# Performance work log

Hardware: AMD Instinct MI355X
Metric: run time of the kernel (lower is better)

The kernel has to match this reference:

```python
import jax, jax.numpy as jnp
import numpy as np

N_NODES = 50000
N_EDGES = 800000
IN, HID, OUT = 128, 128, 64


def _mean_agg(h, src, dst, n):
    # gather source-node features along edges, segment-mean into destination nodes
    msgs = h[src]                                          # [E, d]
    summ = jax.ops.segment_sum(msgs, dst, num_segments=n)  # [N, d]
    deg = jax.ops.segment_sum(jnp.ones((src.shape[0],), h.dtype), dst, num_segments=n)
    return summ / jnp.maximum(deg, 1.0)[:, None]           # zero-in-degree -> 0


def _sage_layer(h, src, dst, W_self, W_neigh, b, n):
    # DGL SAGEConv mean: fc_self(h) + fc_neigh(mean_neigh(h)) + bias
    agg = _mean_agg(h, src, dst, n)
    return h @ W_self + agg @ W_neigh + b


def setup_inputs() -> dict:
    key = jax.random.key(0)
    ks = jax.random.split(key, 8)
    s = 1.0 / np.sqrt(IN)
    return {
        "feat": jax.random.normal(ks[0], (N_NODES, IN), jnp.float32),
        "src": jax.random.randint(ks[1], (N_EDGES,), 0, N_NODES, jnp.int64),
        "dst": jax.random.randint(ks[2], (N_EDGES,), 0, N_NODES, jnp.int64),
        "W_self1": jax.random.normal(ks[3], (IN, HID), jnp.float32) * s,
        "W_neigh1": jax.random.normal(ks[4], (IN, HID), jnp.float32) * s,
        "b1": jnp.zeros((HID,), jnp.float32),
        "W_self2": jax.random.normal(ks[5], (HID, OUT), jnp.float32) * (1.0 / np.sqrt(HID)),
        "W_neigh2": jax.random.normal(ks[6], (HID, OUT), jnp.float32) * (1.0 / np.sqrt(HID)),
        "b2": jnp.zeros((OUT,), jnp.float32),
    }


def reference(feat, src, dst, W_self1, W_neigh1, b1, W_self2, W_neigh2, b2):
    n = feat.shape[0]
    h = _sage_layer(feat, src, dst, W_self1, W_neigh1, b1, n)
    h = jax.nn.relu(h)  # dropout is identity in eval mode
    h = _sage_layer(h, src, dst, W_self2, W_neigh2, b2, n)
    return h
```

## Files before the change

### kernel.cpp

```cpp
#include <hip/hip_runtime.h>

#define N_NODES 50000
#define N_EDGES 800000

typedef unsigned short ushort_t;
typedef unsigned int uint_t;
typedef __attribute__((ext_vector_type(8))) short bf16x8;
typedef __attribute__((ext_vector_type(4))) float f32x4;

#define NB 196
#define BCAP 6144
#define SDEPTH 32
#define EPB 2048
#define NBLK_BUCKET ((N_EDGES + EPB - 1) / EPB)
#define NCVT4 (N_NODES * 128 / 4)

#define IOFF_ROWPTR  100000
#define IOFF_EIDX    150016
#define IOFF_BCNT    950528
#define UOFF_WT      1920000
#define UOFF_FEATB   2000000
#define UOFF_AGG1B   8400000
#define UOFF_H1B     14800000
#define UOFF_P2B     21200000

__device__ __forceinline__ float bf2f(uint_t u) {
    return __uint_as_float(u << 16);
}
__device__ __forceinline__ uint_t f2bf(float f) {
    uint_t x = __float_as_uint(f);
    return (x + 0x7FFFu + ((x >> 16) & 1u)) >> 16;
}

__global__ __launch_bounds__(256) void prep_kernel(const float* __restrict__ feat,
                                                   const float* __restrict__ Ws1,
                                                   const float* __restrict__ Wn1,
                                                   const float* __restrict__ Ws2,
                                                   const float* __restrict__ Wn2,
                                                   ushort_t* __restrict__ featb,
                                                   ushort_t* __restrict__ wT,
                                                   int* __restrict__ bcnt) {
    int i = blockIdx.x * 256 + threadIdx.x;
    if (i < NCVT4) {
        float4 v = ((const float4*)feat)[i];
        uint2 o;
        o.x = f2bf(v.x) | (f2bf(v.y) << 16);
        o.y = f2bf(v.z) | (f2bf(v.w) << 16);
        ((uint2*)featb)[i] = o;
        return;
    }
    int j = i - NCVT4;
    if (j < 49152) {
        float v;
        if (j < 16384) {
            int n = j >> 7, k = j & 127;
            v = Ws1[k * 128 + n];
        } else if (j < 32768) {
            int jj = j - 16384, n = jj >> 7, k = jj & 127;
            v = Wn1[k * 128 + n];
        } else if (j < 40960) {
            int jj = j - 32768, n = jj >> 7, k = jj & 127;
            v = Wn2[k * 64 + n];
        } else {
            int jj = j - 40960, n = jj >> 7, k = jj & 127;
            v = Ws2[k * 64 + n];
        }
        wT[j] = (ushort_t)f2bf(v);
        return;
    }
    int z = j - 49152;
    if (z < NB) bcnt[z] = 0;
}

__global__ __launch_bounds__(256) void bucket_kernel(const int* __restrict__ src,
                                                     const int* __restrict__ dst,
                                                     uint_t* __restrict__ bucket,
                                                     int* __restrict__ bcnt) {
    __shared__ uint_t stage[NB][SDEPTH];
    __shared__ int lcnt[NB];
    __shared__ int gbase[NB];
    int tid = threadIdx.x;
    for (int i = tid; i < NB; i += 256) lcnt[i] = 0;
    __syncthreads();
    int e0 = blockIdx.x * EPB;
#pragma unroll
    for (int it = 0; it < EPB / 256; ++it) {
        int e = e0 + it * 256 + tid;
        if (e < N_EDGES) {
            int d = dst[e], s = src[e];
            uint_t v = ((uint_t)d << 16) | (uint_t)s;
            int b = d >> 8;
            int slot = atomicAdd(&lcnt[b], 1);
            if (slot < SDEPTH) {
                stage[b][slot] = v;
            } else {
                int p = atomicAdd(&bcnt[b], 1);
                bucket[(long)b * BCAP + p] = v;
            }
        }
    }
    __syncthreads();
    if (tid < NB) {
        int n = min(lcnt[tid], SDEPTH);
        gbase[tid] = (n > 0) ? atomicAdd(&bcnt[tid], n) : 0;
    }
    __syncthreads();
    for (int s = tid; s < NB * SDEPTH; s += 256) {
        int b = s >> 5, i = s & (SDEPTH - 1);
        if (i < min(lcnt[b], SDEPTH))
            bucket[(long)b * BCAP + gbase[b] + i] = stage[b][i];
    }
}

__global__ __launch_bounds__(1024) void fill_bucket(const uint_t* __restrict__ bucket,
                                                    const int* __restrict__ bcnt,
                                                    int* __restrict__ rowptr,
                                                    ushort_t* __restrict__ eidx) {
    __shared__ int pref[256];
    __shared__ int hist[256];
    __shared__ int excl[256];
    __shared__ int fp[256];
    int b = blockIdx.x, tid = threadIdx.x;
    if (tid < 256) {
        pref[tid] = (tid < NB) ? bcnt[tid] : 0;
        hist[tid] = 0;
        fp[tid] = 0;
    }
    __syncthreads();
    for (int off = 1; off < 256; off <<= 1) {
        int t = 0;
        if (tid < 256 && tid >= off) t = pref[tid - off];
        __syncthreads();
        if (tid < 256) pref[tid] += t;
        __syncthreads();
    }
    int n = bcnt[b];
    int base = pref[b] - n;
    if (b == NB - 1 && tid == 0) rowptr[N_NODES] = pref[NB - 1];
    int nodebase = b << 8;
    const uint_t* bk = bucket + (long)b * BCAP;
    for (int i = tid; i < n; i += 1024) {
        int d = (int)(bk[i] >> 16) - nodebase;
        atomicAdd(&hist[d], 1);
    }
    __syncthreads();
    int v = 0;
    if (tid < 256) { v = hist[tid]; excl[tid] = v; }
    __syncthreads();
    for (int off = 1; off < 256; off <<= 1) {
        int t = 0;
        if (tid < 256 && tid >= off) t = excl[tid - off];
        __syncthreads();
        if (tid < 256) excl[tid] += t;
        __syncthreads();
    }
    if (tid < 256) {
        excl[tid] -= v;
        int node = nodebase + tid;
        if (node < N_NODES) rowptr[node] = base + excl[tid];
    }
    __syncthreads();
    for (int i = tid; i < n; i += 1024) {
        uint_t vv = bk[i];
        int d = (int)(vv >> 16) - nodebase;
        int off = atomicAdd(&fp[d], 1);
        eidx[base + excl[d] + off] = (ushort_t)(vv & 0xFFFFu);
    }
}

__global__ __launch_bounds__(256) void gather128_kernel(const int* __restrict__ rowptr,
                                                        const ushort_t* __restrict__ eidx,
                                                        const ushort_t* __restrict__ xb,
                                                        ushort_t* __restrict__ aggb) {
    int node = blockIdx.x * 4 + (threadIdx.x >> 6);
    int lane = threadIdx.x & 63;
    if (node >= N_NODES) return;
    int q = lane >> 4;
    int sl = lane & 15;
    int beg = rowptr[node], end = rowptr[node + 1];
    float acc[8];
#pragma unroll
    for (int j = 0; j < 8; ++j) acc[j] = 0.f;

    int e = beg;
    for (; e + 7 < end; e += 8) {
        int sA = eidx[e + q];
        int sB = eidx[e + 4 + q];
        uint4 vA = *(const uint4*)(xb + (long)sA * 128 + sl * 8);
        uint4 vB = *(const uint4*)(xb + (long)sB * 128 + sl * 8);
        acc[0] += bf2f(vA.x & 0xffffu); acc[1] += bf2f(vA.x >> 16);
        acc[2] += bf2f(vA.y & 0xffffu); acc[3] += bf2f(vA.y >> 16);
        acc[4] += bf2f(vA.z & 0xffffu); acc[5] += bf2f(vA.z >> 16);
        acc[6] += bf2f(vA.w & 0xffffu); acc[7] += bf2f(vA.w >> 16);
        acc[0] += bf2f(vB.x & 0xffffu); acc[1] += bf2f(vB.x >> 16);
        acc[2] += bf2f(vB.y & 0xffffu); acc[3] += bf2f(vB.y >> 16);
        acc[4] += bf2f(vB.z & 0xffffu); acc[5] += bf2f(vB.z >> 16);
        acc[6] += bf2f(vB.w & 0xffffu); acc[7] += bf2f(vB.w >> 16);
    }
    for (; e + 3 < end; e += 4) {
        int s = eidx[e + q];
        uint4 v = *(const uint4*)(xb + (long)s * 128 + sl * 8);
        acc[0] += bf2f(v.x & 0xffffu); acc[1] += bf2f(v.x >> 16);
        acc[2] += bf2f(v.y & 0xffffu); acc[3] += bf2f(v.y >> 16);
        acc[4] += bf2f(v.z & 0xffffu); acc[5] += bf2f(v.z >> 16);
        acc[6] += bf2f(v.w & 0xffffu); acc[7] += bf2f(v.w >> 16);
    }
    if (e + q < end) {
        int s = eidx[e + q];
        uint4 v = *(const uint4*)(xb + (long)s * 128 + sl * 8);
        acc[0] += bf2f(v.x & 0xffffu); acc[1] += bf2f(v.x >> 16);
        acc[2] += bf2f(v.y & 0xffffu); acc[3] += bf2f(v.y >> 16);
        acc[4] += bf2f(v.z & 0xffffu); acc[5] += bf2f(v.z >> 16);
        acc[6] += bf2f(v.w & 0xffffu); acc[7] += bf2f(v.w >> 16);
    }
#pragma unroll
    for (int j = 0; j < 8; ++j) {
        acc[j] += __shfl_xor(acc[j], 16);
        acc[j] += __shfl_xor(acc[j], 32);
    }
    float inv = (end > beg) ? 1.0f / (float)(end - beg) : 0.f;
    if (lane < 16) {
        uint4 o;
        o.x = f2bf(acc[0] * inv) | (f2bf(acc[1] * inv) << 16);
        o.y = f2bf(acc[2] * inv) | (f2bf(acc[3] * inv) << 16);
        o.z = f2bf(acc[4] * inv) | (f2bf(acc[5] * inv) << 16);
        o.w = f2bf(acc[6] * inv) | (f2bf(acc[7] * inv) << 16);
        *(uint4*)(aggb + (long)node * 128 + sl * 8) = o;
    }
}

__global__ __launch_bounds__(256) void gather64_add_kernel(const int* __restrict__ rowptr,
                                                           const ushort_t* __restrict__ eidx,
                                                           const ushort_t* __restrict__ p2b,
                                                           float* __restrict__ out) {
    int node = blockIdx.x * 4 + (threadIdx.x >> 6);
    int lane = threadIdx.x & 63;
    if (node >= N_NODES) return;
    int q = lane >> 4;
    int sl = lane & 15;
    int beg = rowptr[node], end = rowptr[node + 1];
    float acc[4];
#pragma unroll
    for (int j = 0; j < 4; ++j) acc[j] = 0.f;

    int e = beg;
    for (; e + 7 < end; e += 8) {
        int sA = eidx[e + q];
        int sB = eidx[e + 4 + q];
        uint2 vA = *(const uint2*)(p2b + (long)sA * 64 + sl * 4);
        uint2 vB = *(const uint2*)(p2b + (long)sB * 64 + sl * 4);
        acc[0] += bf2f(vA.x & 0xffffu); acc[1] += bf2f(vA.x >> 16);
        acc[2] += bf2f(vA.y & 0xffffu); acc[3] += bf2f(vA.y >> 16);
        acc[0] += bf2f(vB.x & 0xffffu); acc[1] += bf2f(vB.x >> 16);
        acc[2] += bf2f(vB.y & 0xffffu); acc[3] += bf2f(vB.y >> 16);
    }
    for (; e + 3 < end; e += 4) {
        int s = eidx[e + q];
        uint2 v = *(const uint2*)(p2b + (long)s * 64 + sl * 4);
        acc[0] += bf2f(v.x & 0xffffu); acc[1] += bf2f(v.x >> 16);
        acc[2] += bf2f(v.y & 0xffffu); acc[3] += bf2f(v.y >> 16);
    }
    if (e + q < end) {
        int s = eidx[e + q];
        uint2 v = *(const uint2*)(p2b + (long)s * 64 + sl * 4);
        acc[0] += bf2f(v.x & 0xffffu); acc[1] += bf2f(v.x >> 16);
        acc[2] += bf2f(v.y & 0xffffu); acc[3] += bf2f(v.y >> 16);
    }
#pragma unroll
    for (int j = 0; j < 4; ++j) {
        acc[j] += __shfl_xor(acc[j], 16);
        acc[j] += __shfl_xor(acc[j], 32);
    }
    float inv = (end > beg) ? 1.0f / (float)(end - beg) : 0.f;
    if (lane < 16) {
        float4* po = (float4*)(out + (long)node * 64 + sl * 4);
        float4 o = *po;
        o.x += acc[0] * inv;
        o.y += acc[1] * inv;
        o.z += acc[2] * inv;
        o.w += acc[3] * inv;
        *po = o;
    }
}


__global__ __launch_bounds__(256) void gemm1_mfma(const ushort_t* __restrict__ featb,
                                                  const ushort_t* __restrict__ agg1b,
                                                  const ushort_t* __restrict__ wT,
                                                  const float* __restrict__ b,
                                                  ushort_t* __restrict__ h1b) {
    int lane = threadIdx.x & 63;
    int w = threadIdx.x >> 6;
    int mbase = blockIdx.x * 128 + w * 32;
    int lr = lane & 15;
    int kg = (lane >> 4) * 8;

    long r0 = mbase + lr;
    long r1 = mbase + 16 + lr;
    if (r0 > N_NODES - 1) r0 = N_NODES - 1;
    if (r1 > N_NODES - 1) r1 = N_NODES - 1;

    f32x4 acc[2][8];
#pragma unroll
    for (int mt = 0; mt < 2; ++mt)
#pragma unroll
        for (int nt = 0; nt < 8; ++nt) acc[mt][nt] = (f32x4){0.f, 0.f, 0.f, 0.f};

#pragma unroll
    for (int pass = 0; pass < 2; ++pass) {
        const ushort_t* a = pass ? agg1b : featb;
        const ushort_t* wt = wT + pass * (128 * 128);
#pragma unroll
        for (int ks = 0; ks < 4; ++ks) {
            int k = ks * 32 + kg;
            bf16x8 a0 = *(const bf16x8*)(a + r0 * 128 + k);
            bf16x8 a1 = *(const bf16x8*)(a + r1 * 128 + k);
#pragma unroll
            for (int nt = 0; nt < 8; ++nt) {
                bf16x8 bb = *(const bf16x8*)(wt + (nt * 16 + lr) * 128 + k);
                acc[0][nt] = __builtin_amdgcn_mfma_f32_16x16x32_bf16(a0, bb, acc[0][nt], 0, 0, 0);
                acc[1][nt] = __builtin_amdgcn_mfma_f32_16x16x32_bf16(a1, bb, acc[1][nt], 0, 0, 0);
            }
        }
    }

    int drow = (lane >> 4) * 4;
#pragma unroll
    for (int nt = 0; nt < 8; ++nt) {
        int n = nt * 16 + lr;
        float bias = b[n];
#pragma unroll
        for (int mt = 0; mt < 2; ++mt) {
#pragma unroll
            for (int r = 0; r < 4; ++r) {
                int row = mbase + mt * 16 + drow + r;
                if (row < N_NODES) {
                    float v = fmaxf(acc[mt][nt][r] + bias, 0.f);
                    h1b[(long)row * 128 + n] = (ushort_t)f2bf(v);
                }
            }
        }
    }
}

__global__ __launch_bounds__(256) void gemm2_mfma(const ushort_t* __restrict__ h1b,
                                                  const ushort_t* __restrict__ wT2,
                                                  const float* __restrict__ b2,
                                                  ushort_t* __restrict__ p2b,
                                                  float* __restrict__ out) {
    int lane = threadIdx.x & 63;
    int w = threadIdx.x >> 6;
    int mbase = blockIdx.x * 128 + w * 32;
    int lr = lane & 15;
    int kg = (lane >> 4) * 8;

    long r0 = mbase + lr;
    long r1 = mbase + 16 + lr;
    if (r0 > N_NODES - 1) r0 = N_NODES - 1;
    if (r1 > N_NODES - 1) r1 = N_NODES - 1;

    f32x4 accP[2][4], accO[2][4];
#pragma unroll
    for (int mt = 0; mt < 2; ++mt)
#pragma unroll
        for (int nt = 0; nt < 4; ++nt) {
            accP[mt][nt] = (f32x4){0.f, 0.f, 0.f, 0.f};
            accO[mt][nt] = (f32x4){0.f, 0.f, 0.f, 0.f};
        }

#pragma unroll
    for (int ks = 0; ks < 4; ++ks) {
        int k = ks * 32 + kg;
        bf16x8 a0 = *(const bf16x8*)(h1b + r0 * 128 + k);
        bf16x8 a1 = *(const bf16x8*)(h1b + r1 * 128 + k);
#pragma unroll
        for (int nt = 0; nt < 4; ++nt) {
            bf16x8 bn = *(const bf16x8*)(wT2 + (nt * 16 + lr) * 128 + k);
            bf16x8 bs = *(const bf16x8*)(wT2 + 8192 + (nt * 16 + lr) * 128 + k);
            accP[0][nt] = __builtin_amdgcn_mfma_f32_16x16x32_bf16(a0, bn, accP[0][nt], 0, 0, 0);
            accP[1][nt] = __builtin_amdgcn_mfma_f32_16x16x32_bf16(a1, bn, accP[1][nt], 0, 0, 0);
            accO[0][nt] = __builtin_amdgcn_mfma_f32_16x16x32_bf16(a0, bs, accO[0][nt], 0, 0, 0);
            accO[1][nt] = __builtin_amdgcn_mfma_f32_16x16x32_bf16(a1, bs, accO[1][nt], 0, 0, 0);
        }
    }

    int drow = (lane >> 4) * 4;
#pragma unroll
    for (int nt = 0; nt < 4; ++nt) {
        int n = nt * 16 + lr;
        float bias = b2[n];
#pragma unroll
        for (int mt = 0; mt < 2; ++mt) {
#pragma unroll
            for (int r = 0; r < 4; ++r) {
                int row = mbase + mt * 16 + drow + r;
                if (row < N_NODES) {
                    p2b[(long)row * 64 + n] = (ushort_t)f2bf(accP[mt][nt][r]);
                    out[(long)row * 64 + n] = accO[mt][nt][r] + bias;
                }
            }
        }
    }
}

extern "C" void kernel_launch(void* const* d_in, const int* in_sizes, int n_in,
                              void* d_out, int out_size, void* d_ws, size_t ws_size,
                              hipStream_t stream) {
    const float* feat = (const float*)d_in[0];
    const int* src    = (const int*)d_in[1];
    const int* dst    = (const int*)d_in[2];
    const float* Ws1  = (const float*)d_in[3];
    const float* Wn1  = (const float*)d_in[4];
    const float* b1   = (const float*)d_in[5];
    const float* Ws2  = (const float*)d_in[6];
    const float* Wn2  = (const float*)d_in[7];
    const float* b2   = (const float*)d_in[8];
    float* out = (float*)d_out;

    int* wsi      = (int*)d_ws;
    ushort_t* wsu = (ushort_t*)d_ws;
    int* rowptr       = wsi + IOFF_ROWPTR;
    ushort_t* eidx    = (ushort_t*)(wsi + IOFF_EIDX);
    int* bcnt         = wsi + IOFF_BCNT;
    ushort_t* wT    = wsu + UOFF_WT;
    ushort_t* featb = wsu + UOFF_FEATB;
    ushort_t* agg1b = wsu + UOFF_AGG1B;
    ushort_t* h1b   = wsu + UOFF_H1B;
    ushort_t* p2b   = wsu + UOFF_P2B;
    uint_t* bucket  = (uint_t*)(wsu + UOFF_H1B);

    prep_kernel<<<(NCVT4 + 49152 + NB + 255) / 256, 256, 0, stream>>>(
        feat, Ws1, Wn1, Ws2, Wn2, featb, wT, bcnt);

    bucket_kernel<<<NBLK_BUCKET, 256, 0, stream>>>(src, dst, bucket, bcnt);
    fill_bucket<<<NB, 1024, 0, stream>>>(bucket, bcnt, rowptr, eidx);

    gather128_kernel<<<(N_NODES + 3) / 4, 256, 0, stream>>>(rowptr, eidx, featb, agg1b);
    gemm1_mfma<<<(N_NODES + 127) / 128, 256, 0, stream>>>(featb, agg1b, wT, b1, h1b);

    gemm2_mfma<<<(N_NODES + 127) / 128, 256, 0, stream>>>(h1b, wT + 32768, b2, p2b, out);
    gather64_add_kernel<<<(N_NODES + 3) / 4, 256, 0, stream>>>(rowptr, eidx, p2b, out);
}
```

Measured before the change: 213.5 us.

## Fuse layer-1 and layer-2 GEMMs through an LDS-resident hidden tile

```diff
diff --git a/kernel.cpp b/kernel.cpp
--- a/kernel.cpp
+++ b/kernel.cpp
@@ -21,7 +21,7 @@
 #define UOFF_WT      1920000
 #define UOFF_FEATB   2000000
 #define UOFF_AGG1B   8400000
-#define UOFF_H1B     14800000
+#define UOFF_BUCKET  14800000
 #define UOFF_P2B     21200000
 
 __device__ __forceinline__ float bf2f(uint_t u) {
@@ -283,17 +283,21 @@
     }
 }
 
-
-__global__ __launch_bounds__(256) void gemm1_mfma(const ushort_t* __restrict__ featb,
-                                                  const ushort_t* __restrict__ agg1b,
-                                                  const ushort_t* __restrict__ wT,
-                                                  const float* __restrict__ b,
-                                                  ushort_t* __restrict__ h1b) {
+__global__ __launch_bounds__(256) void gemm12_mfma(const ushort_t* __restrict__ featb,
+                                                   const ushort_t* __restrict__ agg1b,
+                                                   const ushort_t* __restrict__ wT,
+                                                   const float* __restrict__ b1,
+                                                   const float* __restrict__ b2,
+                                                   ushort_t* __restrict__ p2b,
+                                                   float* __restrict__ out) {
+    __shared__ ushort_t hlds[128][128];
     int lane = threadIdx.x & 63;
     int w = threadIdx.x >> 6;
     int mbase = blockIdx.x * 128 + w * 32;
+    int lbase = w * 32;
     int lr = lane & 15;
     int kg = (lane >> 4) * 8;
+    int drow = (lane >> 4) * 4;
 
     long r0 = mbase + lr;
     long r1 = mbase + 16 + lr;
@@ -324,40 +328,25 @@
         }
     }
 
-    int drow = (lane >> 4) * 4;
 #pragma unroll
     for (int nt = 0; nt < 8; ++nt) {
         int n = nt * 16 + lr;
-        float bias = b[n];
+        float bias = b1[n];
 #pragma unroll
         for (int mt = 0; mt < 2; ++mt) {
 #pragma unroll
             for (int r = 0; r < 4; ++r) {
-                int row = mbase + mt * 16 + drow + r;
-                if (row < N_NODES) {
-                    float v = fmaxf(acc[mt][nt][r] + bias, 0.f);
-                    h1b[(long)row * 128 + n] = (ushort_t)f2bf(v);
-                }
+                int lrow = lbase + mt * 16 + drow + r;
+                float v = fmaxf(acc[mt][nt][r] + bias, 0.f);
+                hlds[lrow][n ^ ((lrow & 7) << 3)] = (ushort_t)f2bf(v);
             }
         }
     }
-}
-
-__global__ __launch_bounds__(256) void gemm2_mfma(const ushort_t* __restrict__ h1b,
-                                                  const ushort_t* __restrict__ wT2,
-                                                  const float* __restrict__ b2,
-                                                  ushort_t* __restrict__ p2b,
-                                                  float* __restrict__ out) {
-    int lane = threadIdx.x & 63;
-    int w = threadIdx.x >> 6;
-    int mbase = blockIdx.x * 128 + w * 32;
-    int lr = lane & 15;
-    int kg = (lane >> 4) * 8;
-
-    long r0 = mbase + lr;
-    long r1 = mbase + 16 + lr;
-    if (r0 > N_NODES - 1) r0 = N_NODES - 1;
-    if (r1 > N_NODES - 1) r1 = N_NODES - 1;
+    __syncthreads();
+
+    const ushort_t* wT2 = wT + 32768;
+    int l0 = lbase + lr;
+    int l1 = lbase + 16 + lr;
 
     f32x4 accP[2][4], accO[2][4];
 #pragma unroll
@@ -371,8 +360,8 @@
 #pragma unroll
     for (int ks = 0; ks < 4; ++ks) {
         int k = ks * 32 + kg;
-        bf16x8 a0 = *(const bf16x8*)(h1b + r0 * 128 + k);
-        bf16x8 a1 = *(const bf16x8*)(h1b + r1 * 128 + k);
+        bf16x8 a0 = *(const bf16x8*)(&hlds[l0][k ^ ((l0 & 7) << 3)]);
+        bf16x8 a1 = *(const bf16x8*)(&hlds[l1][k ^ ((l1 & 7) << 3)]);
 #pragma unroll
         for (int nt = 0; nt < 4; ++nt) {
             bf16x8 bn = *(const bf16x8*)(wT2 + (nt * 16 + lr) * 128 + k);
@@ -384,7 +373,6 @@
         }
     }
 
-    int drow = (lane >> 4) * 4;
 #pragma unroll
     for (int nt = 0; nt < 4; ++nt) {
         int n = nt * 16 + lr;
@@ -425,9 +413,8 @@
     ushort_t* wT    = wsu + UOFF_WT;
     ushort_t* featb = wsu + UOFF_FEATB;
     ushort_t* agg1b = wsu + UOFF_AGG1B;
-    ushort_t* h1b   = wsu + UOFF_H1B;
     ushort_t* p2b   = wsu + UOFF_P2B;
-    uint_t* bucket  = (uint_t*)(wsu + UOFF_H1B);
+    uint_t* bucket  = (uint_t*)(wsu + UOFF_BUCKET);
 
     prep_kernel<<<(NCVT4 + 49152 + NB + 255) / 256, 256, 0, stream>>>(
         feat, Ws1, Wn1, Ws2, Wn2, featb, wT, bcnt);
@@ -436,8 +423,8 @@
     fill_bucket<<<NB, 1024, 0, stream>>>(bucket, bcnt, rowptr, eidx);
 
     gather128_kernel<<<(N_NODES + 3) / 4, 256, 0, stream>>>(rowptr, eidx, featb, agg1b);
-    gemm1_mfma<<<(N_NODES + 127) / 128, 256, 0, stream>>>(featb, agg1b, wT, b1, h1b);
-
-    gemm2_mfma<<<(N_NODES + 127) / 128, 256, 0, stream>>>(h1b, wT + 32768, b2, p2b, out);
+
+    gemm12_mfma<<<(N_NODES + 127) / 128, 256, 0, stream>>>(featb, agg1b, wT, b1, b2, p2b, out);
+
     gather64_add_kernel<<<(N_NODES + 3) / 4, 256, 0, stream>>>(rowptr, eidx, p2b, out);
 }
```

After: 198.7 us. 6.9% less time.
